# Performance work log

Hardware: AMD Instinct MI355X
Metric: run time of the kernel (lower is better)

## Reference

```python
import jax, jax.numpy as jnp
import numpy as np

J = 15       # joints
D = 128      # per-joint feature dim
ANG = 3      # per-joint angle dim
EPS = 1e-12  # F.normalize eps
TEMP = 200.0
SCALE = 16.0


def setup_inputs() -> dict:
    key = jax.random.key(0)
    k1, k2 = jax.random.split(key)
    B, N, E = 16384, 68, J * D + J * ANG  # E = 1965
    emb = jax.random.normal(k1, (B, E), dtype=jnp.float32)
    W = jax.random.normal(k2, (N, E), dtype=jnp.float32)
    return {"emb": emb, "W": W}


def reference(emb, W):
    B = emb.shape[0]
    N = W.shape[0]
    # split feature / angle blocks
    x_feat = emb[:, : J * D].reshape(B, J, D)        # (B, 15, 128)
    x_ang = emb[:, J * D :].reshape(B, 1, J, ANG)    # (B, 1, 15, 3)
    p_feat = W[:, : J * D].reshape(N, J, D)          # (N, 15, 128)
    p_ang = W[:, J * D :].reshape(1, N, J, ANG)      # (1, N, 15, 3)

    # per-joint angle distance and (detached in torch) softmax weighting
    ang_w = jnp.linalg.norm(x_ang - p_ang, axis=-1)            # (B, N, 15)
    w2 = jax.nn.softmax(ang_w / TEMP, axis=-1) * J             # (B, N, 15)

    # NOTE: the torch code computes argsort(ang_w) but immediately overwrites the
    # index with an identity permutation (ind = [0..14]), so the gather is a no-op.
    # Hence normalization is over the flat 15*128 block per batch / per class.
    xn = x_feat / jnp.maximum(
        jnp.linalg.norm(x_feat.reshape(B, -1), axis=-1), EPS
    )[:, None, None]
    pn = p_feat / jnp.maximum(
        jnp.linalg.norm(p_feat.reshape(N, -1), axis=-1), EPS
    )[:, None, None]

    # per-joint cosine contributions, weighted and summed
    s = jnp.einsum("bjd,njd->bnj", xn, pn)                     # (B, N, 15)
    logit = (s * w2).sum(-1) * SCALE                           # (B, N)
    return logit
```

## Files before the change

### kernel.cpp

```cpp
#include <hip/hip_runtime.h>
#include <hip/hip_bf16.h>

typedef __bf16 bf16x8 __attribute__((ext_vector_type(8)));
typedef __bf16 bf16x4 __attribute__((ext_vector_type(4)));
typedef float  f32x4  __attribute__((ext_vector_type(4)));

static constexpr int E    = 1965;
static constexpr int KF   = 1920;
static constexpr int NJ   = 15;
static constexpr int NCLS = 68;
static constexpr int NPAD = 80;
static constexpr int NT   = 5;
static constexpr int NS   = 60;

static constexpr int CH   = 6;
static constexpr int CCOL = 320;
static constexpr int CST  = 10;
static constexpr int SEGS = 80;

static constexpr size_t PNF_BYTES = (size_t)NT * NS * 64 * 8 * 2;

__global__ __launch_bounds__(256) void prep_kernel(const float* __restrict__ W,
                                                   __bf16* __restrict__ pnf,
                                                   float* __restrict__ pa) {
    const int n = blockIdx.x;
    const int t = threadIdx.x;
    float v[8];
    float ss = 0.f;
    if (n < NCLS && t < 240) {
        const float* src = W + (size_t)n * E + 8 * t;
        #pragma unroll
        for (int i = 0; i < 8; ++i) { v[i] = src[i]; ss += v[i] * v[i]; }
    } else {
        #pragma unroll
        for (int i = 0; i < 8; ++i) v[i] = 0.f;
    }
    #pragma unroll
    for (int off = 32; off >= 1; off >>= 1) ss += __shfl_xor(ss, off);
    __shared__ float rbuf[4];
    if ((t & 63) == 0) rbuf[t >> 6] = ss;
    __syncthreads();
    const float total = rbuf[0] + rbuf[1] + rbuf[2] + rbuf[3];
    const float rnorm = 1.f / fmaxf(sqrtf(total), 1e-12f);

    if (t < 240) {
        bf16x8 o;
        #pragma unroll
        for (int i = 0; i < 8; ++i) o[i] = (__bf16)(v[i] * rnorm);
        const int s = t >> 2, g = t & 3;
        const int lane = (n & 15) + 16 * g;
        const size_t off = (((size_t)(n >> 4) * NS + s) * 64 + lane) * 8;
        *(bf16x8*)(pnf + off) = o;
    }
    if (t < 45) {
        pa[n * 45 + t] = (n < NCLS) ? W[(size_t)n * E + KF + t] : 0.f;
    }
}

__global__ __launch_bounds__(320) void cos_kernel(const float* __restrict__ emb,
                                                  const __bf16* __restrict__ pnf,
                                                  const float* __restrict__ pa,
                                                  float* __restrict__ out) {
    __shared__ f32x4  Abuf[2][SEGS][16];
    __shared__ __bf16 pal[NPAD][52];
    __shared__ float  xa[16][48];

    const int tid = threadIdx.x;
    const int m0  = blockIdx.x * 16;
    const int w   = tid >> 6;
    const int l   = tid & 63;
    const int lr  = l & 15;
    const int lg  = l >> 4;

    for (int idx = tid; idx < 16 * 45; idx += 320) {
        const int r = idx / 45, c = idx - r * 45;
        xa[r][c] = emb[(size_t)(m0 + r) * E + KF + c];
    }
    for (int idx = tid; idx < NPAD * 45; idx += 320) {
        const int n = idx / 45, c = idx - n * 45;
        pal[n][c] = (__bf16)pa[idx];
    }
    asm volatile("s_waitcnt lgkmcnt(0)" ::: "memory");

    const float* gbase = emb + (size_t)(m0 + lr) * E + (16 * w + lg) * 4;
    #define ISSUE_CHUNK(c)                                                              \
        {                                                                               \
            const float* g_ = gbase + (c) * CCOL;                                       \
            _Pragma("unroll")                                                           \
            for (int i_ = 0; i_ < 4; ++i_)                                              \
                __builtin_amdgcn_global_load_lds(                                       \
                    (const __attribute__((address_space(1))) void*)(g_ + i_ * 16),      \
                    (__attribute__((address_space(3))) void*)&Abuf[(c) & 1][16 * w + 4 * i_][0], \
                    16, 0, 0);                                                          \
        }

    ISSUE_CHUNK(0);

    const bf16x8* bp = (const bf16x8*)pnf + (size_t)w * NS * 64 + l;

    f32x4 acc[NJ];
    #pragma unroll
    for (int j = 0; j < NJ; ++j) acc[j] = f32x4{0.f, 0.f, 0.f, 0.f};
    float ssq = 0.f;

    #pragma unroll
    for (int c = 0; c < CH; ++c) {
        __builtin_amdgcn_s_barrier();
        if (c + 1 < CH) {
            ISSUE_CHUNK(c + 1);
            asm volatile("s_waitcnt vmcnt(4)" ::: "memory");
        } else {
            asm volatile("s_waitcnt vmcnt(0)" ::: "memory");
        }
        __builtin_amdgcn_s_barrier();

        bf16x8 bfr[CST];
        #pragma unroll
        for (int s = 0; s < CST; ++s) bfr[s] = bp[(c * CST + s) * 64];

        #pragma unroll
        for (int s = 0; s < CST; ++s) {
            const f32x4 alo = Abuf[c & 1][8 * s + 2 * lg][lr];
            const f32x4 ahi = Abuf[c & 1][8 * s + 2 * lg + 1][lr];
            bf16x8 af;
            #pragma unroll
            for (int q = 0; q < 4; ++q) {
                ssq += alo[q] * alo[q];
                ssq += ahi[q] * ahi[q];
                af[q]     = (__bf16)alo[q];
                af[4 + q] = (__bf16)ahi[q];
            }
            acc[(c * CST + s) >> 2] =
                __builtin_amdgcn_mfma_f32_16x16x32_bf16(af, bfr[s], acc[(c * CST + s) >> 2], 0, 0, 0);
        }
    }
    #undef ISSUE_CHUNK

    ssq += __shfl_xor(ssq, 16);
    ssq += __shfl_xor(ssq, 32);

    const int r0  = lg * 4;
    const int col = w * 16 + lr;

    float rn[4];
    #pragma unroll
    for (int r = 0; r < 4; ++r)
        rn[r] = 240.f / fmaxf(sqrtf(__shfl(ssq, r0 + r)), 1e-12f);

    float pr[45];
    #pragma unroll
    for (int q = 0; q < 12; ++q) {
        const bf16x4 pv = *(const bf16x4*)&pal[col][4 * q];
        #pragma unroll
        for (int e = 0; e < 4; ++e)
            if (4 * q + e < 45) pr[4 * q + e] = (float)pv[e];
    }

    float num[4] = {0.f, 0.f, 0.f, 0.f};
    float den[4] = {0.f, 0.f, 0.f, 0.f};
    #pragma unroll
    for (int r = 0; r < 4; ++r) {
        f32x4 xr[12];
        #pragma unroll
        for (int q = 0; q < 12; ++q)
            xr[q] = *(const f32x4*)&xa[r0 + r][4 * q];
        #pragma unroll
        for (int j = 0; j < NJ; ++j) {
            const float d0 = xr[(3 * j + 0) >> 2][(3 * j + 0) & 3] - pr[3 * j + 0];
            const float d1 = xr[(3 * j + 1) >> 2][(3 * j + 1) & 3] - pr[3 * j + 1];
            const float d2 = xr[(3 * j + 2) >> 2][(3 * j + 2) & 3] - pr[3 * j + 2];
            const float dist = sqrtf(d0 * d0 + d1 * d1 + d2 * d2);
            const float e = __expf(dist * 0.005f);
            den[r] += e;
            num[r] += e * acc[j][r];
        }
    }

    if (col < NCLS) {
        #pragma unroll
        for (int r = 0; r < 4; ++r)
            out[(size_t)(m0 + r0 + r) * NCLS + col] = rn[r] * num[r] / den[r];
    }
}

extern "C" void kernel_launch(void* const* d_in, const int* in_sizes, int n_in,
                              void* d_out, int out_size, void* d_ws, size_t ws_size,
                              hipStream_t stream) {
    const float* emb = (const float*)d_in[0];
    const float* W   = (const float*)d_in[1];
    float* out = (float*)d_out;
    __bf16* pnf = (__bf16*)d_ws;
    float*  pa  = (float*)((char*)d_ws + PNF_BYTES);
    const int B = in_sizes[0] / E;

    prep_kernel<<<NPAD, 256, 0, stream>>>(W, pnf, pa);
    cos_kernel<<<B / 16, 320, 0, stream>>>(emb, pnf, pa, out);
}
```

Measured before the change: 84.63 us.

## Deepen emb prefetch pipeline to four smaller LDS buffers with register-double-buffered B

Splits the K loop into 12 smaller chunks of 160 columns and keeps four LDS buffers so up to three chunks of emb are in flight, with one barrier per chunk instead of two. The pnf (B operand) fragments are double-buffered in registers and loaded for the next chunk after the current MFMAs. The aim is to hide global-load latency better in this memory-bound kernel. In exchange it uses more registers and relies on hand-counted vmcnt waits, which makes the code fragile.

```diff
diff --git a/kernel.cpp b/kernel.cpp
--- a/kernel.cpp
+++ b/kernel.cpp
@@ -13,10 +13,11 @@
 static constexpr int NT   = 5;
 static constexpr int NS   = 60;
 
-static constexpr int CH   = 6;
-static constexpr int CCOL = 320;
-static constexpr int CST  = 10;
-static constexpr int SEGS = 80;
+static constexpr int CH   = 12;
+static constexpr int KPC  = 5;
+static constexpr int CCOL = 160;
+static constexpr int SEGC = 40;
+static constexpr int NBUF = 4;
 
 static constexpr size_t PNF_BYTES = (size_t)NT * NS * 64 * 8 * 2;
 
@@ -61,7 +62,7 @@
                                                   const __bf16* __restrict__ pnf,
                                                   const float* __restrict__ pa,
                                                   float* __restrict__ out) {
-    __shared__ f32x4  Abuf[2][SEGS][16];
+    __shared__ f32x4  Abuf[NBUF][SEGC][16];
     __shared__ __bf16 pal[NPAD][52];
     __shared__ float  xa[16][48];
 
@@ -80,21 +81,17 @@
         const int n = idx / 45, c = idx - n * 45;
         pal[n][c] = (__bf16)pa[idx];
     }
-    asm volatile("s_waitcnt lgkmcnt(0)" ::: "memory");
-
-    const float* gbase = emb + (size_t)(m0 + lr) * E + (16 * w + lg) * 4;
-    #define ISSUE_CHUNK(c)                                                              \
+
+    const float* gbase = emb + (size_t)(m0 + lr) * E + 4 * (8 * w + lg);
+    #define ISSUE(c)                                                                    \
         {                                                                               \
-            const float* g_ = gbase + (c) * CCOL;                                       \
             _Pragma("unroll")                                                           \
-            for (int i_ = 0; i_ < 4; ++i_)                                              \
+            for (int i_ = 0; i_ < 2; ++i_)                                              \
                 __builtin_amdgcn_global_load_lds(                                       \
-                    (const __attribute__((address_space(1))) void*)(g_ + i_ * 16),      \
-                    (__attribute__((address_space(3))) void*)&Abuf[(c) & 1][16 * w + 4 * i_][0], \
+                    (const __attribute__((address_space(1))) void*)(gbase + (c) * CCOL + 16 * i_), \
+                    (__attribute__((address_space(3))) void*)&Abuf[(c) & 3][8 * w + 4 * i_][0],    \
                     16, 0, 0);                                                          \
         }
-
-    ISSUE_CHUNK(0);
 
     const bf16x8* bp = (const bf16x8*)pnf + (size_t)w * NS * 64 + l;
 
@@ -103,38 +100,47 @@
     for (int j = 0; j < NJ; ++j) acc[j] = f32x4{0.f, 0.f, 0.f, 0.f};
     float ssq = 0.f;
 
+    bf16x8 bfr[2][KPC];
+    #pragma unroll
+    for (int j = 0; j < KPC; ++j) bfr[0][j] = bp[j * 64];
+
+    ISSUE(0); ISSUE(1); ISSUE(2);
+    asm volatile("s_waitcnt vmcnt(4) lgkmcnt(0)" ::: "memory");
+    __builtin_amdgcn_sched_barrier(0);
+
     #pragma unroll
     for (int c = 0; c < CH; ++c) {
         __builtin_amdgcn_s_barrier();
-        if (c + 1 < CH) {
-            ISSUE_CHUNK(c + 1);
-            asm volatile("s_waitcnt vmcnt(4)" ::: "memory");
-        } else {
-            asm volatile("s_waitcnt vmcnt(0)" ::: "memory");
-        }
-        __builtin_amdgcn_s_barrier();
-
-        bf16x8 bfr[CST];
-        #pragma unroll
-        for (int s = 0; s < CST; ++s) bfr[s] = bp[(c * CST + s) * 64];
-
-        #pragma unroll
-        for (int s = 0; s < CST; ++s) {
-            const f32x4 alo = Abuf[c & 1][8 * s + 2 * lg][lr];
-            const f32x4 ahi = Abuf[c & 1][8 * s + 2 * lg + 1][lr];
+        if (c + 3 < CH) ISSUE(c + 3);
+
+        #pragma unroll
+        for (int j = 0; j < KPC; ++j) {
+            const int s0 = 8 * j + 2 * lg;
+            const f32x4 alo = Abuf[c & 3][s0][lr];
+            const f32x4 ahi = Abuf[c & 3][s0 + 1][lr];
             bf16x8 af;
             #pragma unroll
             for (int q = 0; q < 4; ++q) {
-                ssq += alo[q] * alo[q];
-                ssq += ahi[q] * ahi[q];
+                ssq += alo[q] * alo[q] + ahi[q] * ahi[q];
                 af[q]     = (__bf16)alo[q];
                 af[4 + q] = (__bf16)ahi[q];
             }
-            acc[(c * CST + s) >> 2] =
-                __builtin_amdgcn_mfma_f32_16x16x32_bf16(af, bfr[s], acc[(c * CST + s) >> 2], 0, 0, 0);
-        }
-    }
-    #undef ISSUE_CHUNK
+            const int gk = c * KPC + j;
+            acc[gk >> 2] = __builtin_amdgcn_mfma_f32_16x16x32_bf16(af, bfr[c & 1][j], acc[gk >> 2], 0, 0, 0);
+        }
+
+        if (c <= CH - 4)      { asm volatile("s_waitcnt vmcnt(4)" ::: "memory"); }
+        else if (c == CH - 3) { asm volatile("s_waitcnt vmcnt(2)" ::: "memory"); }
+        else if (c == CH - 2) { asm volatile("s_waitcnt vmcnt(0)" ::: "memory"); }
+        __builtin_amdgcn_sched_barrier(0);
+
+        if (c + 1 < CH) {
+            #pragma unroll
+            for (int j = 0; j < KPC; ++j)
+                bfr[(c + 1) & 1][j] = bp[((c + 1) * KPC + j) * 64];
+        }
+    }
+    #undef ISSUE
 
     ssq += __shfl_xor(ssq, 16);
     ssq += __shfl_xor(ssq, 32);
```

Measured after the change: 89.38 us. 1.06x slower.
